# Kernel tuning notes

Hardware: AMD Instinct MI355X
Metric: run time of the kernel (lower is better)

Reference implementation:

```python
import jax, jax.numpy as jnp
import numpy as np

N_NODES = 100000

def sage_conv(x, edge_index, Wl, bl, Wr):
    # PyG SAGEConv: out = lin_l(mean_agg(x_src -> dst)) + lin_r(x)
    src, dst = edge_index[0], edge_index[1]
    msgs = x[src]                                   # [E, F] gather
    sums = jax.ops.segment_sum(msgs, dst, num_segments=N_NODES)   # [N, F]
    cnt = jax.ops.segment_sum(jnp.ones((edge_index.shape[1],), x.dtype), dst,
                              num_segments=N_NODES)               # [N]
    mean = sums / jnp.maximum(cnt, 1.0)[:, None]
    return mean @ Wl + bl + x @ Wr


def setup_inputs() -> dict:
    key = jax.random.key(0)
    ks = jax.random.split(key, 12)
    in_dim, hid = 32, 64
    x = jax.random.normal(ks[0], (N_NODES, in_dim), dtype=jnp.float32)
    edge_index = jax.random.randint(ks[1], (2, 3200000), 0, N_NODES)
    edge_pairs = jax.random.randint(ks[2], (1000000, 2), 0, N_NODES)
    def lin(k, fi, fo):
        bound = 1.0 / np.sqrt(fi)
        return jax.random.uniform(k, (fi, fo), jnp.float32, -bound, bound)
    params = {
        'Wl1': lin(ks[3], in_dim, hid), 'bl1': jnp.zeros((hid,), jnp.float32),
        'Wr1': lin(ks[4], in_dim, hid),
        'Wl2': lin(ks[5], hid, hid),    'bl2': jnp.zeros((hid,), jnp.float32),
        'Wr2': lin(ks[6], hid, hid),
        'Wh':  lin(ks[7], 2 * hid, 1),  'bh': jnp.zeros((1,), jnp.float32),
    }
    return dict(x=x, edge_index=edge_index, edge_pairs=edge_pairs, **params)


def reference(x, edge_index, edge_pairs, Wl1, bl1, Wr1, Wl2, bl2, Wr2, Wh, bh):
    h = jax.nn.relu(sage_conv(x, edge_index, Wl1, bl1, Wr1))
    h = jax.nn.relu(sage_conv(h, edge_index, Wl2, bl2, Wr2))
    src = h[edge_pairs[:, 0]]
    dst = h[edge_pairs[:, 1]]
    edge_repr = jnp.concatenate([src, dst], axis=1)   # [P, 2*hid]
    logits = (edge_repr @ Wh + bh)[:, 0]              # [P]
    return logits
```

## Files before the change

### kernel.cpp

```cpp
#include <hip/hip_runtime.h>

typedef unsigned int uint;
typedef unsigned short ushort;
typedef __attribute__((ext_vector_type(8))) short bf16x8;
typedef __attribute__((ext_vector_type(4))) float f32x4;

#define N_NODES 100000
#define N_EDGES 3200000
#define N_PAIRS 1000000
#define N_TILES (N_NODES / 16)

#define BUCK_SHIFT 8
#define BUCK_NODES 256
#define NBUCK ((N_NODES + BUCK_NODES - 1) / BUCK_NODES)
#define CAP 8704
#define CH 8192
#define NCHB ((N_EDGES + CH - 1) / CH)
#define EPL (CH / 256)

__device__ __forceinline__ float bf_lo(uint u) { return __uint_as_float(u << 16); }
__device__ __forceinline__ float bf_hi(uint u) { return __uint_as_float(u & 0xFFFF0000u); }
__device__ __forceinline__ ushort f2bf(float f) {
  uint u = __float_as_uint(f);
  return (ushort)((u + 0x7FFF + ((u >> 16) & 1)) >> 16);
}
__device__ __forceinline__ uint pack2bf(float lo, float hi) {
  return (uint)f2bf(lo) | ((uint)f2bf(hi) << 16);
}


__global__ void __launch_bounds__(256) k_prep(
    const float* __restrict__ x,
    const float* __restrict__ Wl1, const float* __restrict__ Wr1,
    const float* __restrict__ Wl2, const float* __restrict__ Wr2,
    ushort* __restrict__ xb, ushort* __restrict__ W1T, ushort* __restrict__ W2T,
    int* __restrict__ woff)
{
  int t = blockIdx.x * blockDim.x + threadIdx.x;
  if (t < N_NODES * 8) {
    float4 f = ((const float4*)x)[t];
    uint2 o;
    o.x = pack2bf(f.x, f.y);
    o.y = pack2bf(f.z, f.w);
    ((uint2*)xb)[t] = o;
  }
  if (t < 4096) {
    int col = t >> 6, f = t & 63;
    float w = (f < 32) ? Wl1[f * 64 + col] : Wr1[(f - 32) * 64 + col];
    W1T[col * 64 + f] = f2bf(w);
  }
  if (t < 8192) {
    int col = t >> 7, f = t & 127;
    float w = (f < 64) ? Wl2[f * 64 + col] : Wr2[(f - 64) * 64 + col];
    W2T[col * 128 + f] = f2bf(w);
  }
  if (t < NBUCK) woff[t] = t * CAP;
}


__global__ void __launch_bounds__(256) k_binning(
    const int* __restrict__ src, const int* __restrict__ dst,
    int* __restrict__ woff, int* __restrict__ bucket_data)
{
  __shared__ uint sorted[CH];
  __shared__ int hist[NBUCK];
  __shared__ int pfx[NBUCK];
  __shared__ int off[NBUCK];
  __shared__ int rbase[NBUCK];
  int t = threadIdx.x;
  int w = t >> 6, lane = t & 63;
  int lo = blockIdx.x * CH;
  int hi = lo + CH; if (hi > N_EDGES) hi = N_EDGES;
  for (int i = t; i < NBUCK; i += 256) hist[i] = 0;
  __syncthreads();
  int dreg[EPL], sreg[EPL];
#pragma unroll
  for (int it = 0; it < EPL; ++it) {
    int e = lo + t + it * 256;
    int dv = -1, sv = 0;
    if (e < hi) { dv = dst[e]; sv = src[e]; }
    dreg[it] = dv; sreg[it] = sv;
    if (dv >= 0) atomicAdd(&hist[dv >> BUCK_SHIFT], 1);
  }
  __syncthreads();
  if (w == 0) {
    int carry = 0;
    for (int c = 0; c < (NBUCK + 63) / 64; ++c) {
      int i = c * 64 + lane;
      int v = (i < NBUCK) ? hist[i] : 0;
      int x = v;
#pragma unroll
      for (int o = 1; o < 64; o <<= 1) {
        int y = __shfl_up(x, o);
        if (lane >= o) x += y;
      }
      if (i < NBUCK) pfx[i] = carry + x - v;
      carry += __shfl(x, 63);
    }
  }
  __syncthreads();
  for (int i = t; i < NBUCK; i += 256) {
    off[i] = pfx[i];
    int h = hist[i];
    rbase[i] = h ? atomicAdd(&woff[i], h) : 0;
  }
  __syncthreads();
#pragma unroll
  for (int it = 0; it < EPL; ++it) {
    int dv = dreg[it];
    if (dv >= 0) {
      int b = dv >> BUCK_SHIFT;
      int slot = atomicAdd(&off[b], 1);
      sorted[slot] = ((uint)sreg[it] << BUCK_SHIFT) | (uint)(dv & (BUCK_NODES - 1));
    }
  }
  __syncthreads();
  for (int b = w; b < NBUCK; b += 4) {
    int h = hist[b];
    int s = pfx[b];
    int g = rbase[b];
    int lim = (b + 1) * CAP - g;
    if (h > lim) h = lim;
    for (int j = lane; j < h; j += 64)
      bucket_data[g + j] = sorted[s + j];
  }
}


__global__ void __launch_bounds__(512) k_bucket_csr(
    const int* __restrict__ woff, const int* __restrict__ bucket_data,
    int* __restrict__ csr, int* __restrict__ row_beg, int* __restrict__ row_end)
{
  __shared__ int hist[BUCK_NODES];
  __shared__ int sc[BUCK_NODES];
  __shared__ int offs[BUCK_NODES];
  int b = blockIdx.x;
  int t = threadIdx.x;
  int base = b * CAP;
  int cnt = woff[b] - base;
  const int* bd = bucket_data + base;
  if (t < BUCK_NODES) hist[t] = 0;
  __syncthreads();
  for (int i = t; i < cnt; i += 512) atomicAdd(&hist[bd[i] & (BUCK_NODES - 1)], 1);
  __syncthreads();
  if (t < BUCK_NODES) sc[t] = hist[t];
  __syncthreads();
  for (int off = 1; off < BUCK_NODES; off <<= 1) {
    int u = 0;
    if (t < BUCK_NODES && t >= off) u = sc[t - off];
    __syncthreads();
    if (t < BUCK_NODES) sc[t] += u;
    __syncthreads();
  }
  if (t < BUCK_NODES) {
    int start = base + sc[t] - hist[t];
    offs[t] = start;
    int node = b * BUCK_NODES + t;
    if (node < N_NODES) { row_beg[node] = start; row_end[node] = start + hist[t]; }
  }
  __syncthreads();
  for (int i = t; i < cnt; i += 512) {
    int pv = bd[i];
    int pos = atomicAdd(&offs[pv & (BUCK_NODES - 1)], 1);
    csr[pos] = pv >> BUCK_SHIFT;
  }
}


__global__ void __launch_bounds__(256) k_gather1(
    const uint4* __restrict__ xb4, const int* __restrict__ row_beg,
    const int* __restrict__ row_end, const int* __restrict__ csr,
    uint4* __restrict__ mean1)
{
  int gid = blockIdx.x * blockDim.x + threadIdx.x;
  int n = gid >> 6;
  int lane = threadIdx.x & 63;
  if (n >= N_NODES) return;
  int slot = lane >> 2;
  int fq = lane & 3;
  int beg = row_beg[n], end = row_end[n];
  int deg = end - beg;
  float s0 = 0.f, s1 = 0.f, s2 = 0.f, s3 = 0.f, s4 = 0.f, s5 = 0.f, s6 = 0.f, s7 = 0.f;
  int i = beg;
  for (; i + 31 < end; i += 32) {
    int n0 = csr[i + slot];
    int n1 = csr[i + 16 + slot];
    uint4 a = xb4[n0 * 4 + fq];
    uint4 b = xb4[n1 * 4 + fq];
    s0 += bf_lo(a.x); s1 += bf_hi(a.x); s2 += bf_lo(a.y); s3 += bf_hi(a.y);
    s4 += bf_lo(a.z); s5 += bf_hi(a.z); s6 += bf_lo(a.w); s7 += bf_hi(a.w);
    s0 += bf_lo(b.x); s1 += bf_hi(b.x); s2 += bf_lo(b.y); s3 += bf_hi(b.y);
    s4 += bf_lo(b.z); s5 += bf_hi(b.z); s6 += bf_lo(b.w); s7 += bf_hi(b.w);
  }
  for (; i < end; i += 16) {
    if (i + slot < end) {
      uint4 a = xb4[csr[i + slot] * 4 + fq];
      s0 += bf_lo(a.x); s1 += bf_hi(a.x); s2 += bf_lo(a.y); s3 += bf_hi(a.y);
      s4 += bf_lo(a.z); s5 += bf_hi(a.z); s6 += bf_lo(a.w); s7 += bf_hi(a.w);
    }
  }
#pragma unroll
  for (int off = 4; off <= 32; off <<= 1) {
    s0 += __shfl_xor(s0, off); s1 += __shfl_xor(s1, off);
    s2 += __shfl_xor(s2, off); s3 += __shfl_xor(s3, off);
    s4 += __shfl_xor(s4, off); s5 += __shfl_xor(s5, off);
    s6 += __shfl_xor(s6, off); s7 += __shfl_xor(s7, off);
  }
  if (slot == 0) {
    float invd = (deg > 0) ? 1.f / (float)deg : 0.f;
    uint4 o;
    o.x = pack2bf(s0 * invd, s1 * invd);
    o.y = pack2bf(s2 * invd, s3 * invd);
    o.z = pack2bf(s4 * invd, s5 * invd);
    o.w = pack2bf(s6 * invd, s7 * invd);
    mean1[n * 4 + fq] = o;
  }
}

__global__ void __launch_bounds__(256) k_gather2(
    const uint4* __restrict__ hb4, const int* __restrict__ row_beg,
    const int* __restrict__ row_end, const int* __restrict__ csr,
    uint4* __restrict__ mean2)
{
  int gid = blockIdx.x * blockDim.x + threadIdx.x;
  int n = gid >> 6;
  int lane = threadIdx.x & 63;
  if (n >= N_NODES) return;
  int slot = lane >> 3;
  int fq = lane & 7;
  int beg = row_beg[n], end = row_end[n];
  int deg = end - beg;
  float s0 = 0.f, s1 = 0.f, s2 = 0.f, s3 = 0.f, s4 = 0.f, s5 = 0.f, s6 = 0.f, s7 = 0.f;
  int i = beg;
  for (; i + 31 < end; i += 32) {
    int n0 = csr[i + slot];
    int n1 = csr[i + 8 + slot];
    int n2 = csr[i + 16 + slot];
    int n3 = csr[i + 24 + slot];
    uint4 a = hb4[n0 * 8 + fq];
    uint4 b = hb4[n1 * 8 + fq];
    uint4 c = hb4[n2 * 8 + fq];
    uint4 d = hb4[n3 * 8 + fq];
    s0 += bf_lo(a.x); s1 += bf_hi(a.x); s2 += bf_lo(a.y); s3 += bf_hi(a.y);
    s4 += bf_lo(a.z); s5 += bf_hi(a.z); s6 += bf_lo(a.w); s7 += bf_hi(a.w);
    s0 += bf_lo(b.x); s1 += bf_hi(b.x); s2 += bf_lo(b.y); s3 += bf_hi(b.y);
    s4 += bf_lo(b.z); s5 += bf_hi(b.z); s6 += bf_lo(b.w); s7 += bf_hi(b.w);
    s0 += bf_lo(c.x); s1 += bf_hi(c.x); s2 += bf_lo(c.y); s3 += bf_hi(c.y);
    s4 += bf_lo(c.z); s5 += bf_hi(c.z); s6 += bf_lo(c.w); s7 += bf_hi(c.w);
    s0 += bf_lo(d.x); s1 += bf_hi(d.x); s2 += bf_lo(d.y); s3 += bf_hi(d.y);
    s4 += bf_lo(d.z); s5 += bf_hi(d.z); s6 += bf_lo(d.w); s7 += bf_hi(d.w);
  }
  for (; i < end; i += 8) {
    if (i + slot < end) {
      uint4 a = hb4[csr[i + slot] * 8 + fq];
      s0 += bf_lo(a.x); s1 += bf_hi(a.x); s2 += bf_lo(a.y); s3 += bf_hi(a.y);
      s4 += bf_lo(a.z); s5 += bf_hi(a.z); s6 += bf_lo(a.w); s7 += bf_hi(a.w);
    }
  }
#pragma unroll
  for (int off = 8; off <= 32; off <<= 1) {
    s0 += __shfl_xor(s0, off); s1 += __shfl_xor(s1, off);
    s2 += __shfl_xor(s2, off); s3 += __shfl_xor(s3, off);
    s4 += __shfl_xor(s4, off); s5 += __shfl_xor(s5, off);
    s6 += __shfl_xor(s6, off); s7 += __shfl_xor(s7, off);
  }
  if (slot == 0) {
    float invd = (deg > 0) ? 1.f / (float)deg : 0.f;
    uint4 o;
    o.x = pack2bf(s0 * invd, s1 * invd);
    o.y = pack2bf(s2 * invd, s3 * invd);
    o.z = pack2bf(s4 * invd, s5 * invd);
    o.w = pack2bf(s6 * invd, s7 * invd);
    mean2[n * 8 + fq] = o;
  }
}


__global__ void __launch_bounds__(256) k_gemm1(
    const ushort* __restrict__ mean1, const ushort* __restrict__ xb,
    const ushort* __restrict__ W1T, const float* __restrict__ bl,
    ushort* __restrict__ h1b)
{
  int wave = (blockIdx.x * blockDim.x + threadIdx.x) >> 6;
  if (wave >= N_TILES) return;
  int lane = threadIdx.x & 63;
  int lc = lane & 15;
  int lg = lane >> 4;
  int n0 = wave * 16;

  bf16x8 bfr[4][2];
#pragma unroll
  for (int j = 0; j < 4; ++j)
#pragma unroll
    for (int kk = 0; kk < 2; ++kk)
      bfr[j][kk] = *(const bf16x8*)(W1T + (j * 16 + lc) * 64 + kk * 32 + lg * 8);

  f32x4 c[4];
#pragma unroll
  for (int j = 0; j < 4; ++j) {
    float b = bl[j * 16 + lc];
    c[j][0] = b; c[j][1] = b; c[j][2] = b; c[j][3] = b;
  }

  bf16x8 a0 = *(const bf16x8*)(mean1 + (n0 + lc) * 32 + lg * 8);
  bf16x8 a1 = *(const bf16x8*)(xb    + (n0 + lc) * 32 + lg * 8);
#pragma unroll
  for (int j = 0; j < 4; ++j) {
    c[j] = __builtin_amdgcn_mfma_f32_16x16x32_bf16(a0, bfr[j][0], c[j], 0, 0, 0);
    c[j] = __builtin_amdgcn_mfma_f32_16x16x32_bf16(a1, bfr[j][1], c[j], 0, 0, 0);
  }

#pragma unroll
  for (int j = 0; j < 4; ++j)
#pragma unroll
    for (int r = 0; r < 4; ++r) {
      int node = n0 + lg * 4 + r;
      h1b[node * 64 + j * 16 + lc] = f2bf(fmaxf(c[j][r], 0.f));
    }
}

__global__ void __launch_bounds__(256) k_gemm2(
    const ushort* __restrict__ mean2, const ushort* __restrict__ h1b,
    const ushort* __restrict__ W2T, const float* __restrict__ bl,
    const float* __restrict__ Wh, float* __restrict__ u, float* __restrict__ v)
{
  int wave = (blockIdx.x * blockDim.x + threadIdx.x) >> 6;
  if (wave >= N_TILES) return;
  int lane = threadIdx.x & 63;
  int lc = lane & 15;
  int lg = lane >> 4;
  int n0 = wave * 16;

  bf16x8 bfr[4][4];
#pragma unroll
  for (int j = 0; j < 4; ++j)
#pragma unroll
    for (int kk = 0; kk < 4; ++kk)
      bfr[j][kk] = *(const bf16x8*)(W2T + (j * 16 + lc) * 128 + kk * 32 + lg * 8);

  f32x4 c[4];
#pragma unroll
  for (int j = 0; j < 4; ++j) {
    float b = bl[j * 16 + lc];
    c[j][0] = b; c[j][1] = b; c[j][2] = b; c[j][3] = b;
  }

  bf16x8 a0 = *(const bf16x8*)(mean2 + (n0 + lc) * 64 + lg * 8);
  bf16x8 a1 = *(const bf16x8*)(mean2 + (n0 + lc) * 64 + 32 + lg * 8);
  bf16x8 a2 = *(const bf16x8*)(h1b   + (n0 + lc) * 64 + lg * 8);
  bf16x8 a3 = *(const bf16x8*)(h1b   + (n0 + lc) * 64 + 32 + lg * 8);
#pragma unroll
  for (int j = 0; j < 4; ++j) {
    c[j] = __builtin_amdgcn_mfma_f32_16x16x32_bf16(a0, bfr[j][0], c[j], 0, 0, 0);
    c[j] = __builtin_amdgcn_mfma_f32_16x16x32_bf16(a1, bfr[j][1], c[j], 0, 0, 0);
    c[j] = __builtin_amdgcn_mfma_f32_16x16x32_bf16(a2, bfr[j][2], c[j], 0, 0, 0);
    c[j] = __builtin_amdgcn_mfma_f32_16x16x32_bf16(a3, bfr[j][3], c[j], 0, 0, 0);
  }

  float pu0 = 0.f, pu1 = 0.f, pu2 = 0.f, pu3 = 0.f;
  float pv0 = 0.f, pv1 = 0.f, pv2 = 0.f, pv3 = 0.f;
#pragma unroll
  for (int j = 0; j < 4; ++j) {
    float wu = Wh[j * 16 + lc];
    float wv = Wh[64 + j * 16 + lc];
    float r0 = fmaxf(c[j][0], 0.f), r1 = fmaxf(c[j][1], 0.f);
    float r2 = fmaxf(c[j][2], 0.f), r3 = fmaxf(c[j][3], 0.f);
    pu0 = fmaf(r0, wu, pu0); pv0 = fmaf(r0, wv, pv0);
    pu1 = fmaf(r1, wu, pu1); pv1 = fmaf(r1, wv, pv1);
    pu2 = fmaf(r2, wu, pu2); pv2 = fmaf(r2, wv, pv2);
    pu3 = fmaf(r3, wu, pu3); pv3 = fmaf(r3, wv, pv3);
  }
#pragma unroll
  for (int off = 1; off <= 8; off <<= 1) {
    pu0 += __shfl_xor(pu0, off); pv0 += __shfl_xor(pv0, off);
    pu1 += __shfl_xor(pu1, off); pv1 += __shfl_xor(pv1, off);
    pu2 += __shfl_xor(pu2, off); pv2 += __shfl_xor(pv2, off);
    pu3 += __shfl_xor(pu3, off); pv3 += __shfl_xor(pv3, off);
  }
  if (lc == 0) {
    int node = n0 + lg * 4;
    u[node]     = pu0; v[node]     = pv0;
    u[node + 1] = pu1; v[node + 1] = pv1;
    u[node + 2] = pu2; v[node + 2] = pv2;
    u[node + 3] = pu3; v[node + 3] = pv3;
  }
}


__global__ void __launch_bounds__(256) k_edge_lite(
    const int2* __restrict__ pairs, const float* __restrict__ u,
    const float* __restrict__ v, const float* __restrict__ bh,
    float* __restrict__ out)
{
  int e = blockIdx.x * blockDim.x + threadIdx.x;
  if (e < N_PAIRS) {
    int2 pr = pairs[e];
    out[e] = u[pr.x] + v[pr.y] + bh[0];
  }
}


extern "C" void kernel_launch(void* const* d_in, const int* in_sizes, int n_in,
                              void* d_out, int out_size, void* d_ws, size_t ws_size,
                              hipStream_t stream)
{
  const float* x   = (const float*)d_in[0];
  const int*   ei  = (const int*)d_in[1];
  const int* pairs = (const int*)d_in[2];
  const float* Wl1 = (const float*)d_in[3];
  const float* bl1 = (const float*)d_in[4];
  const float* Wr1 = (const float*)d_in[5];
  const float* Wl2 = (const float*)d_in[6];
  const float* bl2 = (const float*)d_in[7];
  const float* Wr2 = (const float*)d_in[8];
  const float* Wh  = (const float*)d_in[9];
  const float* bh  = (const float*)d_in[10];
  float* out = (float*)d_out;

  const int* src = ei;
  const int* dst = ei + N_EDGES;

  char* p = (char*)d_ws;
  auto alloc = [&](size_t bytes) {
    char* r = p;
    p += (bytes + 255) & ~(size_t)255;
    return r;
  };
  int*    woff        = (int*)alloc((size_t)NBUCK * 4);
  int*    bucket_data = (int*)alloc((size_t)NBUCK * CAP * 4);
  int*    csr         = (int*)alloc((size_t)NBUCK * CAP * 4);
  int*    row_beg     = (int*)alloc((size_t)N_NODES * 4);
  int*    row_end     = (int*)alloc((size_t)N_NODES * 4);
  ushort* xb          = (ushort*)alloc((size_t)N_NODES * 32 * 2);
  ushort* mean1       = (ushort*)alloc((size_t)N_NODES * 32 * 2);
  ushort* h1b         = (ushort*)alloc((size_t)N_NODES * 64 * 2);
  ushort* W1T         = (ushort*)alloc(64 * 64 * 2);
  ushort* W2T         = (ushort*)alloc(64 * 128 * 2);
  float*  uu          = (float*)alloc((size_t)N_NODES * 4);
  float*  vv          = (float*)alloc((size_t)N_NODES * 4);
  ushort* mean2       = (ushort*)bucket_data;

  k_prep<<<(N_NODES * 8 + 255) / 256, 256, 0, stream>>>(
      x, Wl1, Wr1, Wl2, Wr2, xb, W1T, W2T, woff);
  k_binning<<<NCHB, 256, 0, stream>>>(src, dst, woff, bucket_data);
  k_bucket_csr<<<NBUCK, 512, 0, stream>>>(woff, bucket_data, csr, row_beg, row_end);

  k_gather1<<<(N_NODES * 64) / 256, 256, 0, stream>>>(
      (const uint4*)xb, row_beg, row_end, csr, (uint4*)mean1);
  k_gemm1<<<(N_TILES * 64 + 255) / 256, 256, 0, stream>>>(mean1, xb, W1T, bl1, h1b);
  k_gather2<<<(N_NODES * 64) / 256, 256, 0, stream>>>(
      (const uint4*)h1b, row_beg, row_end, csr, (uint4*)mean2);
  k_gemm2<<<(N_TILES * 64 + 255) / 256, 256, 0, stream>>>(
      mean2, h1b, W2T, bl2, Wh, uu, vv);
  k_edge_lite<<<(N_PAIRS + 255) / 256, 256, 0, stream>>>(
      (const int2*)pairs, uu, vv, bh, out);
}
```

Measured before the change: 208.2 us.

## Fuse neighbor-mean gather with MFMA projection per 16-node block for both layers

Merges each layer's gather kernel and GEMM kernel into one 1024-thread block that handles 16 nodes. Each of 16 waves aggregates one node's neighbor mean into LDS, then 4 waves run the MFMA for one 16-column slice each. This removes the global mean1/mean2 round trips and two launches. In exchange, 12 of 16 waves sit idle during the GEMM phase, and the large blocks with a barrier may hurt occupancy and latency hiding in the gather.

```diff
diff --git a/kernel.cpp b/kernel.cpp
--- a/kernel.cpp
+++ b/kernel.cpp
@@ -8,7 +8,7 @@
 #define N_NODES 100000
 #define N_EDGES 3200000
 #define N_PAIRS 1000000
-#define N_TILES (N_NODES / 16)
+#define NBLK (N_NODES / 16)
 
 #define BUCK_SHIFT 8
 #define BUCK_NODES 256
@@ -167,15 +167,17 @@
 }
 
 
-__global__ void __launch_bounds__(256) k_gather1(
-    const uint4* __restrict__ xb4, const int* __restrict__ row_beg,
-    const int* __restrict__ row_end, const int* __restrict__ csr,
-    uint4* __restrict__ mean1)
-{
-  int gid = blockIdx.x * blockDim.x + threadIdx.x;
-  int n = gid >> 6;
-  int lane = threadIdx.x & 63;
-  if (n >= N_NODES) return;
+__global__ void __launch_bounds__(1024) k_layer1f(
+    const uint4* __restrict__ xb4, const ushort* __restrict__ xb,
+    const int* __restrict__ row_beg, const int* __restrict__ row_end,
+    const int* __restrict__ csr, const ushort* __restrict__ W1T,
+    const float* __restrict__ bl, ushort* __restrict__ h1b)
+{
+  __shared__ uint4 mean_lds[16 * 5];
+  int b = blockIdx.x;
+  int t = threadIdx.x;
+  int w = t >> 6, lane = t & 63;
+  int n = b * 16 + w;
   int slot = lane >> 2;
   int fq = lane & 3;
   int beg = row_beg[n], end = row_end[n];
@@ -186,11 +188,11 @@
     int n0 = csr[i + slot];
     int n1 = csr[i + 16 + slot];
     uint4 a = xb4[n0 * 4 + fq];
-    uint4 b = xb4[n1 * 4 + fq];
+    uint4 bb = xb4[n1 * 4 + fq];
     s0 += bf_lo(a.x); s1 += bf_hi(a.x); s2 += bf_lo(a.y); s3 += bf_hi(a.y);
     s4 += bf_lo(a.z); s5 += bf_hi(a.z); s6 += bf_lo(a.w); s7 += bf_hi(a.w);
-    s0 += bf_lo(b.x); s1 += bf_hi(b.x); s2 += bf_lo(b.y); s3 += bf_hi(b.y);
-    s4 += bf_lo(b.z); s5 += bf_hi(b.z); s6 += bf_lo(b.w); s7 += bf_hi(b.w);
+    s0 += bf_lo(bb.x); s1 += bf_hi(bb.x); s2 += bf_lo(bb.y); s3 += bf_hi(bb.y);
+    s4 += bf_lo(bb.z); s5 += bf_hi(bb.z); s6 += bf_lo(bb.w); s7 += bf_hi(bb.w);
   }
   for (; i < end; i += 16) {
     if (i + slot < end) {
@@ -213,19 +215,42 @@
     o.y = pack2bf(s2 * invd, s3 * invd);
     o.z = pack2bf(s4 * invd, s5 * invd);
     o.w = pack2bf(s6 * invd, s7 * invd);
-    mean1[n * 4 + fq] = o;
-  }
-}
-
-__global__ void __launch_bounds__(256) k_gather2(
-    const uint4* __restrict__ hb4, const int* __restrict__ row_beg,
-    const int* __restrict__ row_end, const int* __restrict__ csr,
-    uint4* __restrict__ mean2)
-{
-  int gid = blockIdx.x * blockDim.x + threadIdx.x;
-  int n = gid >> 6;
-  int lane = threadIdx.x & 63;
-  if (n >= N_NODES) return;
+    mean_lds[w * 5 + fq] = o;
+  }
+  __syncthreads();
+  if (w < 4) {
+    int lc = lane & 15, lg = lane >> 4;
+    bf16x8 bfr0 = *(const bf16x8*)(W1T + (w * 16 + lc) * 64 + lg * 8);
+    bf16x8 bfr1 = *(const bf16x8*)(W1T + (w * 16 + lc) * 64 + 32 + lg * 8);
+    float bb = bl[w * 16 + lc];
+    f32x4 c; c[0] = bb; c[1] = bb; c[2] = bb; c[3] = bb;
+    bf16x8 a0 = *(const bf16x8*)&mean_lds[lc * 5 + lg];
+    bf16x8 a1 = *(const bf16x8*)(xb + (b * 16 + lc) * 32 + lg * 8);
+    c = __builtin_amdgcn_mfma_f32_16x16x32_bf16(a0, bfr0, c, 0, 0, 0);
+    c = __builtin_amdgcn_mfma_f32_16x16x32_bf16(a1, bfr1, c, 0, 0, 0);
+#pragma unroll
+    for (int r = 0; r < 4; ++r) {
+      int node = b * 16 + lg * 4 + r;
+      h1b[node * 64 + w * 16 + lc] = f2bf(fmaxf(c[r], 0.f));
+    }
+  }
+}
+
+
+__global__ void __launch_bounds__(1024) k_layer2f(
+    const uint4* __restrict__ hb4, const ushort* __restrict__ h1b,
+    const int* __restrict__ row_beg, const int* __restrict__ row_end,
+    const int* __restrict__ csr, const ushort* __restrict__ W2T,
+    const float* __restrict__ bl, const float* __restrict__ Wh,
+    float* __restrict__ u, float* __restrict__ v)
+{
+  __shared__ uint4 m2[16 * 9];
+  __shared__ float pu_lds[4 * 16];
+  __shared__ float pv_lds[4 * 16];
+  int b = blockIdx.x;
+  int t = threadIdx.x;
+  int w = t >> 6, lane = t & 63;
+  int n = b * 16 + w;
   int slot = lane >> 3;
   int fq = lane & 7;
   int beg = row_beg[n], end = row_end[n];
@@ -238,13 +263,13 @@
     int n2 = csr[i + 16 + slot];
     int n3 = csr[i + 24 + slot];
     uint4 a = hb4[n0 * 8 + fq];
-    uint4 b = hb4[n1 * 8 + fq];
+    uint4 bb = hb4[n1 * 8 + fq];
     uint4 c = hb4[n2 * 8 + fq];
     uint4 d = hb4[n3 * 8 + fq];
     s0 += bf_lo(a.x); s1 += bf_hi(a.x); s2 += bf_lo(a.y); s3 += bf_hi(a.y);
     s4 += bf_lo(a.z); s5 += bf_hi(a.z); s6 += bf_lo(a.w); s7 += bf_hi(a.w);
-    s0 += bf_lo(b.x); s1 += bf_hi(b.x); s2 += bf_lo(b.y); s3 += bf_hi(b.y);
-    s4 += bf_lo(b.z); s5 += bf_hi(b.z); s6 += bf_lo(b.w); s7 += bf_hi(b.w);
+    s0 += bf_lo(bb.x); s1 += bf_hi(bb.x); s2 += bf_lo(bb.y); s3 += bf_hi(bb.y);
+    s4 += bf_lo(bb.z); s5 += bf_hi(bb.z); s6 += bf_lo(bb.w); s7 += bf_hi(bb.w);
     s0 += bf_lo(c.x); s1 += bf_hi(c.x); s2 += bf_lo(c.y); s3 += bf_hi(c.y);
     s4 += bf_lo(c.z); s5 += bf_hi(c.z); s6 += bf_lo(c.w); s7 += bf_hi(c.w);
     s0 += bf_lo(d.x); s1 += bf_hi(d.x); s2 += bf_lo(d.y); s3 += bf_hi(d.y);
@@ -271,118 +296,52 @@
     o.y = pack2bf(s2 * invd, s3 * invd);
     o.z = pack2bf(s4 * invd, s5 * invd);
     o.w = pack2bf(s6 * invd, s7 * invd);
-    mean2[n * 8 + fq] = o;
-  }
-}
-
-
-__global__ void __launch_bounds__(256) k_gemm1(
-    const ushort* __restrict__ mean1, const ushort* __restrict__ xb,
-    const ushort* __restrict__ W1T, const float* __restrict__ bl,
-    ushort* __restrict__ h1b)
-{
-  int wave = (blockIdx.x * blockDim.x + threadIdx.x) >> 6;
-  if (wave >= N_TILES) return;
-  int lane = threadIdx.x & 63;
-  int lc = lane & 15;
-  int lg = lane >> 4;
-  int n0 = wave * 16;
-
-  bf16x8 bfr[4][2];
-#pragma unroll
-  for (int j = 0; j < 4; ++j)
-#pragma unroll
-    for (int kk = 0; kk < 2; ++kk)
-      bfr[j][kk] = *(const bf16x8*)(W1T + (j * 16 + lc) * 64 + kk * 32 + lg * 8);
-
-  f32x4 c[4];
-#pragma unroll
-  for (int j = 0; j < 4; ++j) {
-    float b = bl[j * 16 + lc];
-    c[j][0] = b; c[j][1] = b; c[j][2] = b; c[j][3] = b;
-  }
-
-  bf16x8 a0 = *(const bf16x8*)(mean1 + (n0 + lc) * 32 + lg * 8);
-  bf16x8 a1 = *(const bf16x8*)(xb    + (n0 + lc) * 32 + lg * 8);
-#pragma unroll
-  for (int j = 0; j < 4; ++j) {
-    c[j] = __builtin_amdgcn_mfma_f32_16x16x32_bf16(a0, bfr[j][0], c[j], 0, 0, 0);
-    c[j] = __builtin_amdgcn_mfma_f32_16x16x32_bf16(a1, bfr[j][1], c[j], 0, 0, 0);
-  }
-
-#pragma unroll
-  for (int j = 0; j < 4; ++j)
-#pragma unroll
-    for (int r = 0; r < 4; ++r) {
-      int node = n0 + lg * 4 + r;
-      h1b[node * 64 + j * 16 + lc] = f2bf(fmaxf(c[j][r], 0.f));
-    }
-}
-
-__global__ void __launch_bounds__(256) k_gemm2(
-    const ushort* __restrict__ mean2, const ushort* __restrict__ h1b,
-    const ushort* __restrict__ W2T, const float* __restrict__ bl,
-    const float* __restrict__ Wh, float* __restrict__ u, float* __restrict__ v)
-{
-  int wave = (blockIdx.x * blockDim.x + threadIdx.x) >> 6;
-  if (wave >= N_TILES) return;
-  int lane = threadIdx.x & 63;
-  int lc = lane & 15;
-  int lg = lane >> 4;
-  int n0 = wave * 16;
-
-  bf16x8 bfr[4][4];
-#pragma unroll
-  for (int j = 0; j < 4; ++j)
-#pragma unroll
-    for (int kk = 0; kk < 4; ++kk)
-      bfr[j][kk] = *(const bf16x8*)(W2T + (j * 16 + lc) * 128 + kk * 32 + lg * 8);
-
-  f32x4 c[4];
-#pragma unroll
-  for (int j = 0; j < 4; ++j) {
-    float b = bl[j * 16 + lc];
-    c[j][0] = b; c[j][1] = b; c[j][2] = b; c[j][3] = b;
-  }
-
-  bf16x8 a0 = *(const bf16x8*)(mean2 + (n0 + lc) * 64 + lg * 8);
-  bf16x8 a1 = *(const bf16x8*)(mean2 + (n0 + lc) * 64 + 32 + lg * 8);
-  bf16x8 a2 = *(const bf16x8*)(h1b   + (n0 + lc) * 64 + lg * 8);
-  bf16x8 a3 = *(const bf16x8*)(h1b   + (n0 + lc) * 64 + 32 + lg * 8);
-#pragma unroll
-  for (int j = 0; j < 4; ++j) {
-    c[j] = __builtin_amdgcn_mfma_f32_16x16x32_bf16(a0, bfr[j][0], c[j], 0, 0, 0);
-    c[j] = __builtin_amdgcn_mfma_f32_16x16x32_bf16(a1, bfr[j][1], c[j], 0, 0, 0);
-    c[j] = __builtin_amdgcn_mfma_f32_16x16x32_bf16(a2, bfr[j][2], c[j], 0, 0, 0);
-    c[j] = __builtin_amdgcn_mfma_f32_16x16x32_bf16(a3, bfr[j][3], c[j], 0, 0, 0);
-  }
-
-  float pu0 = 0.f, pu1 = 0.f, pu2 = 0.f, pu3 = 0.f;
-  float pv0 = 0.f, pv1 = 0.f, pv2 = 0.f, pv3 = 0.f;
-#pragma unroll
-  for (int j = 0; j < 4; ++j) {
-    float wu = Wh[j * 16 + lc];
-    float wv = Wh[64 + j * 16 + lc];
-    float r0 = fmaxf(c[j][0], 0.f), r1 = fmaxf(c[j][1], 0.f);
-    float r2 = fmaxf(c[j][2], 0.f), r3 = fmaxf(c[j][3], 0.f);
-    pu0 = fmaf(r0, wu, pu0); pv0 = fmaf(r0, wv, pv0);
-    pu1 = fmaf(r1, wu, pu1); pv1 = fmaf(r1, wv, pv1);
-    pu2 = fmaf(r2, wu, pu2); pv2 = fmaf(r2, wv, pv2);
-    pu3 = fmaf(r3, wu, pu3); pv3 = fmaf(r3, wv, pv3);
-  }
-#pragma unroll
-  for (int off = 1; off <= 8; off <<= 1) {
-    pu0 += __shfl_xor(pu0, off); pv0 += __shfl_xor(pv0, off);
-    pu1 += __shfl_xor(pu1, off); pv1 += __shfl_xor(pv1, off);
-    pu2 += __shfl_xor(pu2, off); pv2 += __shfl_xor(pv2, off);
-    pu3 += __shfl_xor(pu3, off); pv3 += __shfl_xor(pv3, off);
-  }
-  if (lc == 0) {
-    int node = n0 + lg * 4;
-    u[node]     = pu0; v[node]     = pv0;
-    u[node + 1] = pu1; v[node + 1] = pv1;
-    u[node + 2] = pu2; v[node + 2] = pv2;
-    u[node + 3] = pu3; v[node + 3] = pv3;
+    m2[w * 9 + fq] = o;
+  }
+  __syncthreads();
+  if (w < 4) {
+    int lc = lane & 15, lg = lane >> 4;
+    bf16x8 bfr0 = *(const bf16x8*)(W2T + (w * 16 + lc) * 128 + lg * 8);
+    bf16x8 bfr1 = *(const bf16x8*)(W2T + (w * 16 + lc) * 128 + 32 + lg * 8);
+    bf16x8 bfr2 = *(const bf16x8*)(W2T + (w * 16 + lc) * 128 + 64 + lg * 8);
+    bf16x8 bfr3 = *(const bf16x8*)(W2T + (w * 16 + lc) * 128 + 96 + lg * 8);
+    float bb = bl[w * 16 + lc];
+    f32x4 c; c[0] = bb; c[1] = bb; c[2] = bb; c[3] = bb;
+    bf16x8 a0 = *(const bf16x8*)&m2[lc * 9 + lg];
+    bf16x8 a1 = *(const bf16x8*)&m2[lc * 9 + 4 + lg];
+    bf16x8 a2 = *(const bf16x8*)(h1b + (b * 16 + lc) * 64 + lg * 8);
+    bf16x8 a3 = *(const bf16x8*)(h1b + (b * 16 + lc) * 64 + 32 + lg * 8);
+    c = __builtin_amdgcn_mfma_f32_16x16x32_bf16(a0, bfr0, c, 0, 0, 0);
+    c = __builtin_amdgcn_mfma_f32_16x16x32_bf16(a1, bfr1, c, 0, 0, 0);
+    c = __builtin_amdgcn_mfma_f32_16x16x32_bf16(a2, bfr2, c, 0, 0, 0);
+    c = __builtin_amdgcn_mfma_f32_16x16x32_bf16(a3, bfr3, c, 0, 0, 0);
+    float wu = Wh[w * 16 + lc];
+    float wv = Wh[64 + w * 16 + lc];
+    float r0 = fmaxf(c[0], 0.f), r1 = fmaxf(c[1], 0.f);
+    float r2 = fmaxf(c[2], 0.f), r3 = fmaxf(c[3], 0.f);
+    float pu0 = r0 * wu, pv0 = r0 * wv;
+    float pu1 = r1 * wu, pv1 = r1 * wv;
+    float pu2 = r2 * wu, pv2 = r2 * wv;
+    float pu3 = r3 * wu, pv3 = r3 * wv;
+#pragma unroll
+    for (int off = 1; off <= 8; off <<= 1) {
+      pu0 += __shfl_xor(pu0, off); pv0 += __shfl_xor(pv0, off);
+      pu1 += __shfl_xor(pu1, off); pv1 += __shfl_xor(pv1, off);
+      pu2 += __shfl_xor(pu2, off); pv2 += __shfl_xor(pv2, off);
+      pu3 += __shfl_xor(pu3, off); pv3 += __shfl_xor(pv3, off);
+    }
+    if (lc == 0) {
+      pu_lds[w * 16 + lg * 4 + 0] = pu0; pv_lds[w * 16 + lg * 4 + 0] = pv0;
+      pu_lds[w * 16 + lg * 4 + 1] = pu1; pv_lds[w * 16 + lg * 4 + 1] = pv1;
+      pu_lds[w * 16 + lg * 4 + 2] = pu2; pv_lds[w * 16 + lg * 4 + 2] = pv2;
+      pu_lds[w * 16 + lg * 4 + 3] = pu3; pv_lds[w * 16 + lg * 4 + 3] = pv3;
+    }
+  }
+  __syncthreads();
+  if (t < 16) {
+    int node = b * 16 + t;
+    u[node] = pu_lds[t] + pu_lds[16 + t] + pu_lds[32 + t] + pu_lds[48 + t];
+    v[node] = pv_lds[t] + pv_lds[16 + t] + pv_lds[32 + t] + pv_lds[48 + t];
   }
 }
 
@@ -432,26 +391,21 @@
   int*    row_beg     = (int*)alloc((size_t)N_NODES * 4);
   int*    row_end     = (int*)alloc((size_t)N_NODES * 4);
   ushort* xb          = (ushort*)alloc((size_t)N_NODES * 32 * 2);
-  ushort* mean1       = (ushort*)alloc((size_t)N_NODES * 32 * 2);
   ushort* h1b         = (ushort*)alloc((size_t)N_NODES * 64 * 2);
   ushort* W1T         = (ushort*)alloc(64 * 64 * 2);
   ushort* W2T         = (ushort*)alloc(64 * 128 * 2);
   float*  uu          = (float*)alloc((size_t)N_NODES * 4);
   float*  vv          = (float*)alloc((size_t)N_NODES * 4);
-  ushort* mean2       = (ushort*)bucket_data;
 
   k_prep<<<(N_NODES * 8 + 255) / 256, 256, 0, stream>>>(
       x, Wl1, Wr1, Wl2, Wr2, xb, W1T, W2T, woff);
   k_binning<<<NCHB, 256, 0, stream>>>(src, dst, woff, bucket_data);
   k_bucket_csr<<<NBUCK, 512, 0, stream>>>(woff, bucket_data, csr, row_beg, row_end);
 
-  k_gather1<<<(N_NODES * 64) / 256, 256, 0, stream>>>(
-      (const uint4*)xb, row_beg, row_end, csr, (uint4*)mean1);
-  k_gemm1<<<(N_TILES * 64 + 255) / 256, 256, 0, stream>>>(mean1, xb, W1T, bl1, h1b);
-  k_gather2<<<(N_NODES * 64) / 256, 256, 0, stream>>>(
-      (const uint4*)h1b, row_beg, row_end, csr, (uint4*)mean2);
-  k_gemm2<<<(N_TILES * 64 + 255) / 256, 256, 0, stream>>>(
-      mean2, h1b, W2T, bl2, Wh, uu, vv);
+  k_layer1f<<<NBLK, 1024, 0, stream>>>(
+      (const uint4*)xb, xb, row_beg, row_end, csr, W1T, bl1, h1b);
+  k_layer2f<<<NBLK, 1024, 0, stream>>>(
+      (const uint4*)h1b, h1b, row_beg, row_end, csr, W2T, bl2, Wh, uu, vv);
   k_edge_lite<<<(N_PAIRS + 255) / 256, 256, 0, stream>>>(
       (const int2*)pairs, uu, vv, bh, out);
 }
```

Measured after the change: 226.1 us. 1.09x slower.
